# Optimization experiments

Hardware: AMD Instinct MI355X
Metric: run time of the kernel (lower is better)

The kernel has to match this reference:

```python
import jax, jax.numpy as jnp
import numpy as np

N_NODES = 100000
N_EDGES = 1600000
D_IN = 128
D_HID = 128
D_OUT = 64


def setup_inputs() -> dict:
    key = jax.random.key(0)
    ks = jax.random.split(key, 8)
    x = jax.random.normal(ks[0], (N_NODES, D_IN), dtype=jnp.float32)
    edge_index = jax.random.randint(ks[1], (2, N_EDGES), 0, N_NODES, dtype=jnp.int64)
    s1 = 1.0 / np.sqrt(D_IN)
    s2 = 1.0 / np.sqrt(D_HID)
    W1 = jax.random.uniform(ks[2], (D_IN, D_HID), jnp.float32, -s1, s1)
    b1 = jnp.zeros((D_HID,), jnp.float32)
    W2 = jax.random.uniform(ks[3], (D_HID, D_HID), jnp.float32, -s2, s2)
    b2 = jnp.zeros((D_HID,), jnp.float32)
    fc_W = jax.random.uniform(ks[4], (D_HID, D_OUT), jnp.float32, -s2, s2)
    fc_b = jax.random.uniform(ks[5], (D_OUT,), jnp.float32, -s2, s2)
    return {"x": x, "edge_index": edge_index, "W1": W1, "b1": b1,
            "W2": W2, "b2": b2, "fc_W": fc_W, "fc_b": fc_b}


def _gcn_norm(edge_index, n_nodes):
    # add self-loops, compute symmetric normalization D^{-1/2} A D^{-1/2}
    loops = jnp.arange(n_nodes, dtype=edge_index.dtype)
    src = jnp.concatenate([edge_index[0], loops])  # [E+N]
    dst = jnp.concatenate([edge_index[1], loops])
    ones = jnp.ones(src.shape[0], jnp.float32)
    deg = jax.ops.segment_sum(ones, dst, num_segments=n_nodes)  # [N]
    dinv = 1.0 / jnp.sqrt(deg)  # deg >= 1 thanks to self-loops
    norm = dinv[src] * dinv[dst]  # [E+N]
    return src, dst, norm


def _gcn_conv(x, W, b, src, dst, norm, n_nodes):
    h = x @ W                                  # [N, d]
    msg = h[src] * norm[:, None]               # gather + scale, [E+N, d]
    out = jax.ops.segment_sum(msg, dst, num_segments=n_nodes)  # scatter-add
    return out + b


def reference(x, edge_index, W1, b1, W2, b2, fc_W, fc_b):
    n = x.shape[0]
    src, dst, norm = _gcn_norm(edge_index, n)
    h = jax.nn.relu(_gcn_conv(x, W1, b1, src, dst, norm, n))
    # dropout is identity in inference mode
    h = jax.nn.relu(_gcn_conv(h, W2, b2, src, dst, norm, n))
    return h @ fc_W + fc_b
```

## Files before the change

kernel.cpp:

```cpp
#include <hip/hip_runtime.h>

typedef __attribute__((ext_vector_type(8))) short bf16x8;
typedef __attribute__((ext_vector_type(4))) float f32x4;
typedef __attribute__((ext_vector_type(2))) float f32x2;

__device__ __forceinline__ unsigned short f2bf(float x) {
  union { float f; unsigned u; } v; v.f = x;
  return (unsigned short)((v.u + 0x7fffu + ((v.u >> 16) & 1u)) >> 16);
}


__global__ __launch_bounds__(256) void bhist_k(const int* __restrict__ dst,
                                               int* __restrict__ bcnt, int E, int B) {
  __shared__ int h[512];
  for (int i = threadIdx.x; i < B; i += 256) h[i] = 0;
  __syncthreads();
  for (int e = blockIdx.x * 256 + threadIdx.x; e < E; e += gridDim.x * 256)
    atomicAdd(&h[dst[e] >> 8], 1);
  __syncthreads();
  for (int i = threadIdx.x; i < B; i += 256)
    if (h[i]) atomicAdd(&bcnt[i * 16], h[i]);
}

__global__ __launch_bounds__(256) void bin_k(const int* __restrict__ src,
                                             const int* __restrict__ dst,
                                             const int* __restrict__ bcnt,
                                             int* __restrict__ bfill,
                                             unsigned* __restrict__ ebuf, int E, int B) {
  __shared__ int hist[512];
  __shared__ int base[512];
  __shared__ int sd[256];
  int t = threadIdx.x;
  int i0 = 2 * t, i1 = 2 * t + 1;
  int v0 = (i0 < B) ? bcnt[i0 * 16] : 0;
  int v1 = (i1 < B) ? bcnt[i1 * 16] : 0;
  int ts = v0 + v1;
  sd[t] = ts; __syncthreads();
  for (int off = 1; off < 256; off <<= 1) {
    int x = (t >= off) ? sd[t - off] : 0;
    __syncthreads();
    sd[t] += x;
    __syncthreads();
  }
  int excl = sd[t] - ts;
  base[i0] = excl;
  base[i1] = excl + v0;
  __syncthreads();

  int chunk = (E + gridDim.x - 1) / gridDim.x;
  int e0 = blockIdx.x * chunk;
  int e1 = e0 + chunk; if (e1 > E) e1 = E;
  for (int i = t; i < B; i += 256) hist[i] = 0;
  __syncthreads();
  for (int e = e0 + t; e < e1; e += 256) atomicAdd(&hist[dst[e] >> 8], 1);
  __syncthreads();
  for (int i = t; i < B; i += 256) {
    int c = hist[i];
    hist[i] = base[i] + (c ? atomicAdd(&bfill[i * 16], c) : 0);
  }
  __syncthreads();
  for (int e = e0 + t; e < e1; e += 256) {
    int d = dst[e];
    int b = d >> 8;
    int pos = atomicAdd(&hist[b], 1);
    ebuf[pos] = ((unsigned)(d & 255) << 17) | (unsigned)src[e];
  }
}

__global__ __launch_bounds__(256) void bsort_k(const unsigned* __restrict__ ebuf,
                                               const int* __restrict__ bcnt,
                                               int* __restrict__ csr,
                                               int* __restrict__ row_start,
                                               float* __restrict__ dinv, int N, int B, int E) {
  __shared__ int cnt[256];
  __shared__ int sd[256];
  __shared__ int ofs[256];
  __shared__ int sorted[8192];
  __shared__ int s_bs, s_m;
  int b = blockIdx.x, t = threadIdx.x;
  int i0 = 2 * t, i1 = 2 * t + 1;
  int v0 = (i0 < B) ? bcnt[i0 * 16] : 0;
  int v1 = (i1 < B) ? bcnt[i1 * 16] : 0;
  int ts = v0 + v1;
  sd[t] = ts; __syncthreads();
  for (int off = 1; off < 256; off <<= 1) {
    int x = (t >= off) ? sd[t - off] : 0;
    __syncthreads();
    sd[t] += x;
    __syncthreads();
  }
  int excl = sd[t] - ts;
  if (i0 == b) { s_bs = excl; s_m = v0; }
  if (i1 == b) { s_bs = excl + v0; s_m = v1; }
  if (b == 0 && t == 0) row_start[N] = E;
  __syncthreads();
  int bs = s_bs, m = s_m;
  if (m > 8192) m = 8192;

  cnt[t] = 0;
  __syncthreads();
  for (int i = t; i < m; i += 256) atomicAdd(&cnt[ebuf[bs + i] >> 17], 1);
  __syncthreads();
  int deg = cnt[t];
  sd[t] = deg; __syncthreads();
  for (int off = 1; off < 256; off <<= 1) {
    int x = (t >= off) ? sd[t - off] : 0;
    __syncthreads();
    sd[t] += x;
    __syncthreads();
  }
  int nexcl = sd[t] - deg;
  ofs[t] = nexcl;
  int node = (b << 8) + t;
  if (node < N) {
    row_start[node] = bs + nexcl;
    dinv[node] = rsqrtf((float)(deg + 1));
  }
  __syncthreads();
  for (int i = t; i < m; i += 256) {
    unsigned r = ebuf[bs + i];
    int d = r >> 17;
    int p = atomicAdd(&ofs[d], 1);
    if (p < 8192) sorted[p] = (int)(r & 0x1FFFFu);
  }
  __syncthreads();
  for (int i = t; i < m; i += 256) csr[bs + i] = sorted[i];
}

template <int NCOL, bool INF32, bool OUTF32, bool SCALE>
__global__ __launch_bounds__(256) void gemm_k(const void* __restrict__ Ap,
                                              const float* __restrict__ W,
                                              const float* __restrict__ bias,
                                              const float* __restrict__ rowscale,
                                              void* __restrict__ Cp, int M) {
  __shared__ __align__(16) unsigned short Ws[NCOL * 136];
  int tid = threadIdx.x;
  for (int e = tid; e < 128 * NCOL; e += 256) {
    int k = e / NCOL, n = e % NCOL;
    Ws[n * 136 + k] = f2bf(W[e]);
  }
  __syncthreads();

  int wave = tid >> 6, lane = tid & 63;
  int q = lane >> 4, r = lane & 15;
  const int NT = NCOL / 16;
  int ntile = M >> 4;
  for (int tile = blockIdx.x * 4 + wave; tile < ntile; tile += gridDim.x * 4) {
    int row = tile * 16 + r;
    bf16x8 a[4];
    if (INF32) {
      const float* A = (const float*)Ap + (size_t)row * 128 + q * 8;
#pragma unroll
      for (int kk = 0; kk < 4; kk++) {
        const float4* p = (const float4*)(A + kk * 32);
        float4 f0 = p[0], f1 = p[1];
        bf16x8 tt;
        tt[0] = (short)f2bf(f0.x); tt[1] = (short)f2bf(f0.y);
        tt[2] = (short)f2bf(f0.z); tt[3] = (short)f2bf(f0.w);
        tt[4] = (short)f2bf(f1.x); tt[5] = (short)f2bf(f1.y);
        tt[6] = (short)f2bf(f1.z); tt[7] = (short)f2bf(f1.w);
        a[kk] = tt;
      }
    } else {
      const unsigned short* A = (const unsigned short*)Ap + (size_t)row * 128 + q * 8;
#pragma unroll
      for (int kk = 0; kk < 4; kk++) a[kk] = *(const bf16x8*)(A + kk * 32);
    }
    f32x4 acc[NT];
#pragma unroll
    for (int nt = 0; nt < NT; nt++) { acc[nt][0] = 0.f; acc[nt][1] = 0.f; acc[nt][2] = 0.f; acc[nt][3] = 0.f; }
#pragma unroll
    for (int kk = 0; kk < 4; kk++) {
#pragma unroll
      for (int nt = 0; nt < NT; nt++) {
        bf16x8 bfr = *(const bf16x8*)&Ws[(nt * 16 + r) * 136 + kk * 32 + q * 8];
        acc[nt] = __builtin_amdgcn_mfma_f32_16x16x32_bf16(a[kk], bfr, acc[nt], 0, 0, 0);
      }
    }
#pragma unroll
    for (int rr = 0; rr < 4; rr++) {
      int orow = tile * 16 + q * 4 + rr;
      float rs = SCALE ? rowscale[orow] : 1.f;
#pragma unroll
      for (int nt = 0; nt < NT; nt++) {
        int ocol = nt * 16 + r;
        if (OUTF32)
          ((float*)Cp)[(size_t)orow * NCOL + ocol] = acc[nt][rr] + bias[ocol];
        else
          ((unsigned short*)Cp)[(size_t)orow * NCOL + ocol] = f2bf(acc[nt][rr] * rs);
      }
    }
  }
}

__global__ __launch_bounds__(256) void agg_k(const unsigned short* __restrict__ hs,
                                             const float* __restrict__ dinv,
                                             const int* __restrict__ row_start,
                                             const int* __restrict__ csr,
                                             const float* __restrict__ bias,
                                             unsigned short* __restrict__ out, int N) {
  int lane = threadIdx.x & 63;
  int node = (blockIdx.x * 256 + threadIdx.x) >> 6;
  if (node >= N) return;
  int g = lane >> 4, r = lane & 15;
  float di = dinv[node];
  int beg = row_start[node];
  int deg = row_start[node + 1] - beg;

  f32x2 acc2[4];
#pragma unroll
  for (int i = 0; i < 4; i++) { acc2[i][0] = 0.f; acc2[i][1] = 0.f; }

#define ACCADD(U)                                                              \
  {                                                                            \
    f32x2 p;                                                                   \
    p[0] = __uint_as_float((U).x << 16);                                       \
    p[1] = __uint_as_float((U).x & 0xffff0000u); acc2[0] += p;                 \
    p[0] = __uint_as_float((U).y << 16);                                       \
    p[1] = __uint_as_float((U).y & 0xffff0000u); acc2[1] += p;                 \
    p[0] = __uint_as_float((U).z << 16);                                       \
    p[1] = __uint_as_float((U).z & 0xffff0000u); acc2[2] += p;                 \
    p[0] = __uint_as_float((U).w << 16);                                       \
    p[1] = __uint_as_float((U).w & 0xffff0000u); acc2[3] += p;                 \
  }
#define ACCFMA(U, M)                                                           \
  {                                                                            \
    f32x2 w2; w2[0] = (M); w2[1] = (M);                                        \
    f32x2 p;                                                                   \
    p[0] = __uint_as_float((U).x << 16);                                       \
    p[1] = __uint_as_float((U).x & 0xffff0000u); acc2[0] += p * w2;            \
    p[0] = __uint_as_float((U).y << 16);                                       \
    p[1] = __uint_as_float((U).y & 0xffff0000u); acc2[1] += p * w2;            \
    p[0] = __uint_as_float((U).z << 16);                                       \
    p[1] = __uint_as_float((U).z & 0xffff0000u); acc2[2] += p * w2;            \
    p[0] = __uint_as_float((U).w << 16);                                       \
    p[1] = __uint_as_float((U).w & 0xffff0000u); acc2[3] += p * w2;            \
  }

  for (int base = -1; base < deg; base += 64) {
    int idx = base + lane;
    int s = node;
    if (idx >= 0 && idx < deg) s = csr[beg + idx];
    int cntv = deg - base; if (cntv > 64) cntv = 64;
    int j = 0;
    for (; j + 8 <= cntv; j += 8) {
      int s0 = __shfl(s, j + g);
      int s1 = __shfl(s, j + 4 + g);
      uint4 u0 = *(const uint4*)(hs + (size_t)s0 * 128 + r * 8);
      uint4 u1 = *(const uint4*)(hs + (size_t)s1 * 128 + r * 8);
      ACCADD(u0); ACCADD(u1);
    }
    for (; j < cntv; j += 4) {
      int sj = __shfl(s, j + g);
      float mk = (j + g < cntv) ? 1.f : 0.f;
      uint4 u = *(const uint4*)(hs + (size_t)sj * 128 + r * 8);
      ACCFMA(u, mk);
    }
  }
#undef ACCADD
#undef ACCFMA

  float a[8];
#pragma unroll
  for (int d = 0; d < 4; d++) { a[2 * d] = acc2[d][0]; a[2 * d + 1] = acc2[d][1]; }
#pragma unroll
  for (int i = 0; i < 8; i++) {
    a[i] += __shfl_xor(a[i], 16);
    a[i] += __shfl_xor(a[i], 32);
  }

  if (g == 0) {
    bf16x8 t;
#pragma unroll
    for (int i = 0; i < 8; i++) {
      float v = a[i] * di + bias[r * 8 + i];
      if (v < 0.f) v = 0.f;
      t[i] = (short)f2bf(v);
    }
    *(bf16x8*)(out + (size_t)node * 128 + r * 8) = t;
  }
}

extern "C" void kernel_launch(void* const* d_in, const int* in_sizes, int n_in,
                              void* d_out, int out_size, void* d_ws, size_t ws_size,
                              hipStream_t stream) {
  const float* x  = (const float*)d_in[0];
  const int* ei   = (const int*)d_in[1];
  const float* W1 = (const float*)d_in[2];
  const float* b1 = (const float*)d_in[3];
  const float* W2 = (const float*)d_in[4];
  const float* b2 = (const float*)d_in[5];
  const float* fcW = (const float*)d_in[6];
  const float* fcb = (const float*)d_in[7];
  float* out = (float*)d_out;

  int N = in_sizes[0] / 128;
  int E = in_sizes[1] / 2;
  int B = (N + 255) >> 8;
  const int* src = ei;
  const int* dst = ei + E;

  char* w = (char*)d_ws;
  auto alloc = [&](size_t b) { char* p = w; w += (b + 255) & ~(size_t)255; return p; };
  float* dinv      = (float*)alloc((size_t)N * 4);
  int*   row_start = (int*)alloc((size_t)(N + 1) * 4);
  int*   batom     = (int*)alloc((size_t)(B + 1) * 128);
  int*   bcnt      = batom;
  int*   bfill     = batom + (size_t)(B + 1) * 16;
  unsigned* ebuf   = (unsigned*)alloc((size_t)E * 4);
  int*   csr       = (int*)alloc((size_t)E * 4);
  unsigned short* bufA = (unsigned short*)alloc((size_t)N * 128 * 2);
  unsigned short* bufB = (unsigned short*)alloc((size_t)N * 128 * 2);

  hipMemsetAsync(batom, 0, (size_t)(B + 1) * 128, stream);

  bhist_k<<<256, 256, 0, stream>>>(dst, bcnt, E, B);
  bin_k<<<256, 256, 0, stream>>>(src, dst, bcnt, bfill, ebuf, E, B);
  bsort_k<<<B, 256, 0, stream>>>(ebuf, bcnt, csr, row_start, dinv, N, B, E);

  gemm_k<128, true, false, true><<<782, 256, 0, stream>>>((const void*)x, W1, nullptr, dinv,
                                                          (void*)bufA, N);
  agg_k<<<(N + 3) / 4, 256, 0, stream>>>(bufA, dinv, row_start, csr, b1, bufB, N);
  gemm_k<128, false, false, true><<<782, 256, 0, stream>>>((const void*)bufB, W2, nullptr, dinv,
                                                           (void*)bufA, N);
  agg_k<<<(N + 3) / 4, 256, 0, stream>>>(bufA, dinv, row_start, csr, b2, bufB, N);
  gemm_k<64, false, true, false><<<782, 256, 0, stream>>>((const void*)bufB, fcW, fcb, nullptr,
                                                          (void*)out, N);
}
```

Baseline: 335.4 us.

## Remap aggregation so each lane owns two columns and batch sixteen neighbor loads

The aggregation kernel now has each lane own two feature columns of the node row, loading 4 bytes per neighbor, instead of four lane groups each loading 16-byte chunks from different neighbors and reducing across groups with shuffles at the end. Neighbor indices are broadcast with readlane and sixteen loads are issued before accumulating, which gives more memory-level parallelism. The final cross-group shuffle reduction goes away. In exchange each load is narrower (4 bytes per lane rather than 16), which means more load instructions per byte, and the tail iteration processes up to sixteen masked neighbors.

New measurement: 333.9 us. Within noise of the previous version (-0.4%).

```diff
diff --git a/kernel.cpp b/kernel.cpp
--- a/kernel.cpp
+++ b/kernel.cpp
@@ -202,40 +202,13 @@
   int lane = threadIdx.x & 63;
   int node = (blockIdx.x * 256 + threadIdx.x) >> 6;
   if (node >= N) return;
-  int g = lane >> 4, r = lane & 15;
   float di = dinv[node];
   int beg = row_start[node];
   int deg = row_start[node + 1] - beg;
 
-  f32x2 acc2[4];
-#pragma unroll
-  for (int i = 0; i < 4; i++) { acc2[i][0] = 0.f; acc2[i][1] = 0.f; }
-
-#define ACCADD(U)                                                              \
-  {                                                                            \
-    f32x2 p;                                                                   \
-    p[0] = __uint_as_float((U).x << 16);                                       \
-    p[1] = __uint_as_float((U).x & 0xffff0000u); acc2[0] += p;                 \
-    p[0] = __uint_as_float((U).y << 16);                                       \
-    p[1] = __uint_as_float((U).y & 0xffff0000u); acc2[1] += p;                 \
-    p[0] = __uint_as_float((U).z << 16);                                       \
-    p[1] = __uint_as_float((U).z & 0xffff0000u); acc2[2] += p;                 \
-    p[0] = __uint_as_float((U).w << 16);                                       \
-    p[1] = __uint_as_float((U).w & 0xffff0000u); acc2[3] += p;                 \
-  }
-#define ACCFMA(U, M)                                                           \
-  {                                                                            \
-    f32x2 w2; w2[0] = (M); w2[1] = (M);                                        \
-    f32x2 p;                                                                   \
-    p[0] = __uint_as_float((U).x << 16);                                       \
-    p[1] = __uint_as_float((U).x & 0xffff0000u); acc2[0] += p * w2;            \
-    p[0] = __uint_as_float((U).y << 16);                                       \
-    p[1] = __uint_as_float((U).y & 0xffff0000u); acc2[1] += p * w2;            \
-    p[0] = __uint_as_float((U).z << 16);                                       \
-    p[1] = __uint_as_float((U).z & 0xffff0000u); acc2[2] += p * w2;            \
-    p[0] = __uint_as_float((U).w << 16);                                       \
-    p[1] = __uint_as_float((U).w & 0xffff0000u); acc2[3] += p * w2;            \
-  }
+  const unsigned short* colp = hs + lane * 2;
+
+  f32x2 acc; acc[0] = 0.f; acc[1] = 0.f;
 
   for (int base = -1; base < deg; base += 64) {
     int idx = base + lane;
@@ -243,42 +216,48 @@
     if (idx >= 0 && idx < deg) s = csr[beg + idx];
     int cntv = deg - base; if (cntv > 64) cntv = 64;
     int j = 0;
-    for (; j + 8 <= cntv; j += 8) {
-      int s0 = __shfl(s, j + g);
-      int s1 = __shfl(s, j + 4 + g);
-      uint4 u0 = *(const uint4*)(hs + (size_t)s0 * 128 + r * 8);
-      uint4 u1 = *(const uint4*)(hs + (size_t)s1 * 128 + r * 8);
-      ACCADD(u0); ACCADD(u1);
-    }
-    for (; j < cntv; j += 4) {
-      int sj = __shfl(s, j + g);
-      float mk = (j + g < cntv) ? 1.f : 0.f;
-      uint4 u = *(const uint4*)(hs + (size_t)sj * 128 + r * 8);
-      ACCFMA(u, mk);
-    }
-  }
-#undef ACCADD
-#undef ACCFMA
-
-  float a[8];
-#pragma unroll
-  for (int d = 0; d < 4; d++) { a[2 * d] = acc2[d][0]; a[2 * d + 1] = acc2[d][1]; }
-#pragma unroll
-  for (int i = 0; i < 8; i++) {
-    a[i] += __shfl_xor(a[i], 16);
-    a[i] += __shfl_xor(a[i], 32);
-  }
-
-  if (g == 0) {
-    bf16x8 t;
-#pragma unroll
-    for (int i = 0; i < 8; i++) {
-      float v = a[i] * di + bias[r * 8 + i];
-      if (v < 0.f) v = 0.f;
-      t[i] = (short)f2bf(v);
-    }
-    *(bf16x8*)(out + (size_t)node * 128 + r * 8) = t;
-  }
+    for (; j + 16 <= cntv; j += 16) {
+      unsigned u[16];
+#pragma unroll
+      for (int k = 0; k < 16; k++) {
+        int sj = __builtin_amdgcn_readlane(s, j + k);
+        u[k] = *(const unsigned*)(colp + (size_t)sj * 128);
+      }
+#pragma unroll
+      for (int k = 0; k < 16; k++) {
+        f32x2 p;
+        p[0] = __uint_as_float(u[k] << 16);
+        p[1] = __uint_as_float(u[k] & 0xffff0000u);
+        acc += p;
+      }
+    }
+    if (j < cntv) {
+      unsigned u[16];
+      float w[16];
+#pragma unroll
+      for (int k = 0; k < 16; k++) {
+        int sj = __builtin_amdgcn_readlane(s, (j + k) & 63);
+        u[k] = *(const unsigned*)(colp + (size_t)sj * 128);
+        w[k] = (j + k < cntv) ? 1.f : 0.f;
+      }
+#pragma unroll
+      for (int k = 0; k < 16; k++) {
+        f32x2 p;
+        p[0] = __uint_as_float(u[k] << 16);
+        p[1] = __uint_as_float(u[k] & 0xffff0000u);
+        f32x2 wv; wv[0] = w[k]; wv[1] = w[k];
+        acc += p * wv;
+      }
+    }
+  }
+
+  f32x2 bv = *(const f32x2*)(bias + lane * 2);
+  float v0 = acc[0] * di + bv[0];
+  float v1 = acc[1] * di + bv[1];
+  if (v0 < 0.f) v0 = 0.f;
+  if (v1 < 0.f) v1 = 0.f;
+  unsigned pk = ((unsigned)f2bf(v1) << 16) | (unsigned)f2bf(v0);
+  *(unsigned*)(out + (size_t)node * 128 + lane * 2) = pk;
 }
 
 extern "C" void kernel_launch(void* const* d_in, const int* in_sizes, int n_in,
```

## Aggregate before second GEMM and fuse GEMM2 with final FC layer

Applied to the files above, without the earlier changes.

Uses the identity A(hW) = (Ah)W to run the second aggregation on pre-scaled layer-1 outputs, with the dinv scaling folded into agg1's output. A single fused kernel then does the W2 GEMM with bias and ReLU and keeps the result in shared memory for the FC GEMM. This removes one kernel launch and a full N x 128 intermediate write and read to global memory. Shared memory use per block grows to about 64KB with XOR-swizzled layouts, which may reduce occupancy, and bf16 rounding happens at different points than before.

Result: slower. 343.7 us (+2.5%).

```diff
diff --git a/kernel.cpp b/kernel.cpp
--- a/kernel.cpp
+++ b/kernel.cpp
@@ -127,52 +127,43 @@
   for (int i = t; i < m; i += 256) csr[bs + i] = sorted[i];
 }
 
-template <int NCOL, bool INF32, bool OUTF32, bool SCALE>
-__global__ __launch_bounds__(256) void gemm_k(const void* __restrict__ Ap,
-                                              const float* __restrict__ W,
-                                              const float* __restrict__ bias,
-                                              const float* __restrict__ rowscale,
-                                              void* __restrict__ Cp, int M) {
-  __shared__ __align__(16) unsigned short Ws[NCOL * 136];
+__global__ __launch_bounds__(256) void gemm1_k(const float* __restrict__ Ap,
+                                               const float* __restrict__ W,
+                                               const float* __restrict__ rowscale,
+                                               unsigned short* __restrict__ Cp, int M) {
+  __shared__ __align__(16) unsigned short Ws[128 * 136];
   int tid = threadIdx.x;
-  for (int e = tid; e < 128 * NCOL; e += 256) {
-    int k = e / NCOL, n = e % NCOL;
+  for (int e = tid; e < 128 * 128; e += 256) {
+    int k = e / 128, n = e % 128;
     Ws[n * 136 + k] = f2bf(W[e]);
   }
   __syncthreads();
 
   int wave = tid >> 6, lane = tid & 63;
   int q = lane >> 4, r = lane & 15;
-  const int NT = NCOL / 16;
   int ntile = M >> 4;
   for (int tile = blockIdx.x * 4 + wave; tile < ntile; tile += gridDim.x * 4) {
     int row = tile * 16 + r;
     bf16x8 a[4];
-    if (INF32) {
-      const float* A = (const float*)Ap + (size_t)row * 128 + q * 8;
-#pragma unroll
-      for (int kk = 0; kk < 4; kk++) {
-        const float4* p = (const float4*)(A + kk * 32);
-        float4 f0 = p[0], f1 = p[1];
-        bf16x8 tt;
-        tt[0] = (short)f2bf(f0.x); tt[1] = (short)f2bf(f0.y);
-        tt[2] = (short)f2bf(f0.z); tt[3] = (short)f2bf(f0.w);
-        tt[4] = (short)f2bf(f1.x); tt[5] = (short)f2bf(f1.y);
-        tt[6] = (short)f2bf(f1.z); tt[7] = (short)f2bf(f1.w);
-        a[kk] = tt;
-      }
-    } else {
-      const unsigned short* A = (const unsigned short*)Ap + (size_t)row * 128 + q * 8;
-#pragma unroll
-      for (int kk = 0; kk < 4; kk++) a[kk] = *(const bf16x8*)(A + kk * 32);
-    }
-    f32x4 acc[NT];
-#pragma unroll
-    for (int nt = 0; nt < NT; nt++) { acc[nt][0] = 0.f; acc[nt][1] = 0.f; acc[nt][2] = 0.f; acc[nt][3] = 0.f; }
+    const float* A = Ap + (size_t)row * 128 + q * 8;
 #pragma unroll
     for (int kk = 0; kk < 4; kk++) {
-#pragma unroll
-      for (int nt = 0; nt < NT; nt++) {
+      const float4* p = (const float4*)(A + kk * 32);
+      float4 f0 = p[0], f1 = p[1];
+      bf16x8 tt;
+      tt[0] = (short)f2bf(f0.x); tt[1] = (short)f2bf(f0.y);
+      tt[2] = (short)f2bf(f0.z); tt[3] = (short)f2bf(f0.w);
+      tt[4] = (short)f2bf(f1.x); tt[5] = (short)f2bf(f1.y);
+      tt[6] = (short)f2bf(f1.z); tt[7] = (short)f2bf(f1.w);
+      a[kk] = tt;
+    }
+    f32x4 acc[8];
+#pragma unroll
+    for (int nt = 0; nt < 8; nt++) { acc[nt][0] = 0.f; acc[nt][1] = 0.f; acc[nt][2] = 0.f; acc[nt][3] = 0.f; }
+#pragma unroll
+    for (int kk = 0; kk < 4; kk++) {
+#pragma unroll
+      for (int nt = 0; nt < 8; nt++) {
         bf16x8 bfr = *(const bf16x8*)&Ws[(nt * 16 + r) * 136 + kk * 32 + q * 8];
         acc[nt] = __builtin_amdgcn_mfma_f32_16x16x32_bf16(a[kk], bfr, acc[nt], 0, 0, 0);
       }
@@ -180,25 +171,107 @@
 #pragma unroll
     for (int rr = 0; rr < 4; rr++) {
       int orow = tile * 16 + q * 4 + rr;
-      float rs = SCALE ? rowscale[orow] : 1.f;
-#pragma unroll
-      for (int nt = 0; nt < NT; nt++) {
+      float rs = rowscale[orow];
+#pragma unroll
+      for (int nt = 0; nt < 8; nt++) {
         int ocol = nt * 16 + r;
-        if (OUTF32)
-          ((float*)Cp)[(size_t)orow * NCOL + ocol] = acc[nt][rr] + bias[ocol];
-        else
-          ((unsigned short*)Cp)[(size_t)orow * NCOL + ocol] = f2bf(acc[nt][rr] * rs);
-      }
-    }
-  }
-}
-
-__global__ __launch_bounds__(256) void agg_k(const unsigned short* __restrict__ hs,
-                                             const float* __restrict__ dinv,
-                                             const int* __restrict__ row_start,
-                                             const int* __restrict__ csr,
-                                             const float* __restrict__ bias,
-                                             unsigned short* __restrict__ out, int N) {
+        Cp[(size_t)orow * 128 + ocol] = f2bf(acc[nt][rr] * rs);
+      }
+    }
+  }
+}
+
+__device__ __forceinline__ int swz(int row, int col) {
+  return row * 128 + (col ^ ((row & 7) << 3));
+}
+
+__global__ __launch_bounds__(256) void gemm2fc_k(const unsigned short* __restrict__ g2,
+                                                 const float* __restrict__ W2,
+                                                 const float* __restrict__ b2,
+                                                 const float* __restrict__ dinv,
+                                                 const float* __restrict__ fcW,
+                                                 const float* __restrict__ fcb,
+                                                 float* __restrict__ out, int M) {
+  __shared__ __align__(16) unsigned short Wa[128 * 128];
+  __shared__ __align__(16) unsigned short Wf[64 * 128];
+  __shared__ __align__(16) unsigned short Ht[4][16 * 128];
+  int tid = threadIdx.x;
+  for (int e = tid; e < 128 * 128; e += 256) {
+    int k = e / 128, n = e % 128;
+    Wa[swz(n, k)] = f2bf(W2[e]);
+  }
+  for (int e = tid; e < 128 * 64; e += 256) {
+    int k = e / 64, n = e % 64;
+    Wf[swz(n, k)] = f2bf(fcW[e]);
+  }
+  __syncthreads();
+
+  int wave = tid >> 6, lane = tid & 63;
+  int q = lane >> 4, r = lane & 15;
+  int ntile = M >> 4;
+  for (int tile = blockIdx.x * 4 + wave; tile < ntile; tile += gridDim.x * 4) {
+    int row = tile * 16 + r;
+    bf16x8 a[4];
+    const unsigned short* A = g2 + (size_t)row * 128 + q * 8;
+#pragma unroll
+    for (int kk = 0; kk < 4; kk++) a[kk] = *(const bf16x8*)(A + kk * 32);
+
+    f32x4 acc[8];
+#pragma unroll
+    for (int nt = 0; nt < 8; nt++) { acc[nt][0] = 0.f; acc[nt][1] = 0.f; acc[nt][2] = 0.f; acc[nt][3] = 0.f; }
+#pragma unroll
+    for (int kk = 0; kk < 4; kk++) {
+#pragma unroll
+      for (int nt = 0; nt < 8; nt++) {
+        bf16x8 bfr = *(const bf16x8*)&Wa[swz(nt * 16 + r, kk * 32 + q * 8)];
+        acc[nt] = __builtin_amdgcn_mfma_f32_16x16x32_bf16(a[kk], bfr, acc[nt], 0, 0, 0);
+      }
+    }
+#pragma unroll
+    for (int rr = 0; rr < 4; rr++) {
+      int orow = tile * 16 + q * 4 + rr;
+      float rs = dinv[orow];
+#pragma unroll
+      for (int nt = 0; nt < 8; nt++) {
+        int col = nt * 16 + r;
+        float v = acc[nt][rr] * rs + b2[col];
+        if (v < 0.f) v = 0.f;
+        Ht[wave][swz(q * 4 + rr, col)] = f2bf(v);
+      }
+    }
+    bf16x8 h[4];
+#pragma unroll
+    for (int kk = 0; kk < 4; kk++)
+      h[kk] = *(const bf16x8*)&Ht[wave][swz(r, kk * 32 + q * 8)];
+    f32x4 accF[4];
+#pragma unroll
+    for (int nt = 0; nt < 4; nt++) { accF[nt][0] = 0.f; accF[nt][1] = 0.f; accF[nt][2] = 0.f; accF[nt][3] = 0.f; }
+#pragma unroll
+    for (int kk = 0; kk < 4; kk++) {
+#pragma unroll
+      for (int nt = 0; nt < 4; nt++) {
+        bf16x8 bfr = *(const bf16x8*)&Wf[swz(nt * 16 + r, kk * 32 + q * 8)];
+        accF[nt] = __builtin_amdgcn_mfma_f32_16x16x32_bf16(h[kk], bfr, accF[nt], 0, 0, 0);
+      }
+    }
+#pragma unroll
+    for (int rr = 0; rr < 4; rr++) {
+      int orow = tile * 16 + q * 4 + rr;
+#pragma unroll
+      for (int nt = 0; nt < 4; nt++) {
+        int ocol = nt * 16 + r;
+        out[(size_t)orow * 64 + ocol] = accF[nt][rr] + fcb[ocol];
+      }
+    }
+  }
+}
+
+__global__ __launch_bounds__(256) void agg1_k(const unsigned short* __restrict__ hs,
+                                              const float* __restrict__ dinv,
+                                              const int* __restrict__ row_start,
+                                              const int* __restrict__ csr,
+                                              const float* __restrict__ bias,
+                                              unsigned short* __restrict__ out, int N) {
   int lane = threadIdx.x & 63;
   int node = (blockIdx.x * 256 + threadIdx.x) >> 6;
   if (node >= N) return;
@@ -257,8 +330,6 @@
       ACCFMA(u, mk);
     }
   }
-#undef ACCADD
-#undef ACCFMA
 
   float a[8];
 #pragma unroll
@@ -275,8 +346,63 @@
     for (int i = 0; i < 8; i++) {
       float v = a[i] * di + bias[r * 8 + i];
       if (v < 0.f) v = 0.f;
-      t[i] = (short)f2bf(v);
-    }
+      t[i] = (short)f2bf(v * di);
+    }
+    *(bf16x8*)(out + (size_t)node * 128 + r * 8) = t;
+  }
+}
+
+__global__ __launch_bounds__(256) void agg2_k(const unsigned short* __restrict__ hs,
+                                              const int* __restrict__ row_start,
+                                              const int* __restrict__ csr,
+                                              unsigned short* __restrict__ out, int N) {
+  int lane = threadIdx.x & 63;
+  int node = (blockIdx.x * 256 + threadIdx.x) >> 6;
+  if (node >= N) return;
+  int g = lane >> 4, r = lane & 15;
+  int beg = row_start[node];
+  int deg = row_start[node + 1] - beg;
+
+  f32x2 acc2[4];
+#pragma unroll
+  for (int i = 0; i < 4; i++) { acc2[i][0] = 0.f; acc2[i][1] = 0.f; }
+
+  for (int base = -1; base < deg; base += 64) {
+    int idx = base + lane;
+    int s = node;
+    if (idx >= 0 && idx < deg) s = csr[beg + idx];
+    int cntv = deg - base; if (cntv > 64) cntv = 64;
+    int j = 0;
+    for (; j + 8 <= cntv; j += 8) {
+      int s0 = __shfl(s, j + g);
+      int s1 = __shfl(s, j + 4 + g);
+      uint4 u0 = *(const uint4*)(hs + (size_t)s0 * 128 + r * 8);
+      uint4 u1 = *(const uint4*)(hs + (size_t)s1 * 128 + r * 8);
+      ACCADD(u0); ACCADD(u1);
+    }
+    for (; j < cntv; j += 4) {
+      int sj = __shfl(s, j + g);
+      float mk = (j + g < cntv) ? 1.f : 0.f;
+      uint4 u = *(const uint4*)(hs + (size_t)sj * 128 + r * 8);
+      ACCFMA(u, mk);
+    }
+  }
+#undef ACCADD
+#undef ACCFMA
+
+  float a[8];
+#pragma unroll
+  for (int d = 0; d < 4; d++) { a[2 * d] = acc2[d][0]; a[2 * d + 1] = acc2[d][1]; }
+#pragma unroll
+  for (int i = 0; i < 8; i++) {
+    a[i] += __shfl_xor(a[i], 16);
+    a[i] += __shfl_xor(a[i], 32);
+  }
+
+  if (g == 0) {
+    bf16x8 t;
+#pragma unroll
+    for (int i = 0; i < 8; i++) t[i] = (short)f2bf(a[i]);
     *(bf16x8*)(out + (size_t)node * 128 + r * 8) = t;
   }
 }
@@ -318,12 +444,8 @@
   bin_k<<<256, 256, 0, stream>>>(src, dst, bcnt, bfill, ebuf, E, B);
   bsort_k<<<B, 256, 0, stream>>>(ebuf, bcnt, csr, row_start, dinv, N, B, E);
 
-  gemm_k<128, true, false, true><<<782, 256, 0, stream>>>((const void*)x, W1, nullptr, dinv,
-                                                          (void*)bufA, N);
-  agg_k<<<(N + 3) / 4, 256, 0, stream>>>(bufA, dinv, row_start, csr, b1, bufB, N);
-  gemm_k<128, false, false, true><<<782, 256, 0, stream>>>((const void*)bufB, W2, nullptr, dinv,
-                                                           (void*)bufA, N);
-  agg_k<<<(N + 3) / 4, 256, 0, stream>>>(bufA, dinv, row_start, csr, b2, bufB, N);
-  gemm_k<64, false, true, false><<<782, 256, 0, stream>>>((const void*)bufB, fcW, fcb, nullptr,
-                                                          (void*)out, N);
-}
+  gemm1_k<<<782, 256, 0, stream>>>(x, W1, dinv, bufA, N);
+  agg1_k<<<(N + 3) / 4, 256, 0, stream>>>(bufA, dinv, row_start, csr, b1, bufB, N);
+  agg2_k<<<(N + 3) / 4, 256, 0, stream>>>(bufB, row_start, csr, bufA, N);
+  gemm2fc_k<<<782, 256, 0, stream>>>(bufA, W2, b2, dinv, fcW, fcb, out, N);
+}
```
